# Kernel tuning notes

Hardware: AMD Instinct MI355X
Metric: run time of the kernel (lower is better)

The kernel has to match this reference:

```python
import jax, jax.numpy as jnp
import numpy as np

N = 50000          # nodes
E = 800000         # edges
F_IN, H, OUT = 512, 256, 2
BN_EPS = 1e-5


def setup_inputs() -> dict:
    key = jax.random.key(0)
    ks = jax.random.split(key, 10)
    x = jax.random.normal(ks[0], (N, F_IN), jnp.float32)
    edge_index = jax.random.randint(ks[1], (2, E), 0, N, dtype=jnp.int64)
    edge_weight = jax.random.uniform(ks[2], (E,), jnp.float32)

    def lin(k, fan_in, fan_out):
        return jax.random.normal(k, (fan_in, fan_out), jnp.float32) / np.sqrt(fan_in).astype(np.float32)

    W1, b1 = lin(ks[3], F_IN, H), jnp.zeros((H,), jnp.float32)
    W2, b2 = lin(ks[4], H, H), jnp.zeros((H,), jnp.float32)
    W3, b3 = lin(ks[5], H, OUT), jnp.zeros((OUT,), jnp.float32)
    # BatchNorm1d affine params + running stats (eval mode)
    g1, be1 = jnp.ones((H,), jnp.float32), jnp.zeros((H,), jnp.float32)
    m1 = 0.1 * jax.random.normal(ks[6], (H,), jnp.float32)
    v1 = jax.random.uniform(ks[7], (H,), jnp.float32, 0.5, 1.5)
    g2, be2 = jnp.ones((H,), jnp.float32), jnp.zeros((H,), jnp.float32)
    m2 = 0.1 * jax.random.normal(ks[8], (H,), jnp.float32)
    v2 = jax.random.uniform(ks[9], (H,), jnp.float32, 0.5, 1.5)
    return {"x": x, "edge_index": edge_index, "edge_weight": edge_weight,
            "W1": W1, "b1": b1, "g1": g1, "be1": be1, "m1": m1, "v1": v1,
            "W2": W2, "b2": b2, "g2": g2, "be2": be2, "m2": m2, "v2": v2,
            "W3": W3, "b3": b3}


def gcn_conv(x, row, col, w, W, b):
    # PyG GCNConv (eval): h = x @ W; out[col] += norm * h[row]; + b
    # row/col/w already include self-loops with weight 1.
    n = x.shape[0]
    h = x @ W                                      # [N, out]
    deg = jax.ops.segment_sum(w, col, num_segments=n)
    dinv = jnp.where(deg > 0, jax.lax.rsqrt(deg), 0.0)
    norm = dinv[row] * w * dinv[col]               # [E+N]
    out = jax.ops.segment_sum(h[row] * norm[:, None], col, num_segments=n)
    return out + b


def batchnorm_eval(x, g, be, m, v):
    return (x - m) * jax.lax.rsqrt(v + BN_EPS) * g + be


def reference(x, edge_index, edge_weight, W1, b1, g1, be1, m1, v1,
              W2, b2, g2, be2, m2, v2, W3, b3):
    n = x.shape[0]
    loops = jnp.arange(n, dtype=edge_index.dtype)
    row = jnp.concatenate([edge_index[0], loops])
    col = jnp.concatenate([edge_index[1], loops])
    w = jnp.concatenate([edge_weight, jnp.ones((n,), x.dtype)])

    h = jax.nn.relu(batchnorm_eval(gcn_conv(x, row, col, w, W1, b1), g1, be1, m1, v1))
    h = jax.nn.relu(batchnorm_eval(gcn_conv(h, row, col, w, W2, b2), g2, be2, m2, v2))
    return gcn_conv(h, row, col, w, W3, b3)
```

## Files before the change

### kernel.cpp

```cpp
#include <hip/hip_runtime.h>
#include <stdint.h>

#define F_IN 512
#define HF 256
#define OUT_F 2
#define BN_EPS 1e-5f
#define SCAN_B 256
#define LDSTR 36

typedef __attribute__((ext_vector_type(8))) short bf16x8;
typedef __attribute__((ext_vector_type(4))) float f32x4;

__device__ inline float bf2f(unsigned short u) {
    union { float f; uint32_t i; } v; v.i = ((uint32_t)u) << 16; return v.f;
}
__device__ inline unsigned short f2bf(float f) {
    union { float f; uint32_t i; } v; v.f = f;
    uint32_t r = v.i + 0x7FFFu + ((v.i >> 16) & 1u);
    return (unsigned short)(r >> 16);
}

__global__ void prep_kernel(unsigned long long* __restrict__ packed,
                            const float* __restrict__ W1, unsigned short* __restrict__ W1t,
                            const float* __restrict__ W2, unsigned short* __restrict__ W2t,
                            unsigned short* __restrict__ xbf_pad,
                            unsigned short* __restrict__ bufa_pad,
                            int n, int padx, int pada) {
    int idx = blockIdx.x * blockDim.x + threadIdx.x;
    if (idx < n) { packed[idx] = 1ULL << 20; return; }
    int j = idx - n;
    if (j < F_IN * HF) {
        int nn = j >> 9, k = j & (F_IN - 1);
        W1t[j] = f2bf(W1[(size_t)k * HF + nn]);
        return;
    }
    j -= F_IN * HF;
    if (j < HF * HF) {
        int nn = j >> 8, k = j & (HF - 1);
        W2t[j] = f2bf(W2[(size_t)k * HF + nn]);
        return;
    }
    j -= HF * HF;
    if (j < padx) { xbf_pad[j] = 0; return; }
    j -= padx;
    if (j < pada) bufa_pad[j] = 0;
}

__global__ void count_conv_kernel(const int* __restrict__ col,
                                  const float* __restrict__ w,
                                  unsigned long long* __restrict__ packed,
                                  const float* __restrict__ x,
                                  unsigned short* __restrict__ xbf,
                                  int e, int nchunk) {
    int tid = blockIdx.x * blockDim.x + threadIdx.x;
    if (tid < e) {
        unsigned long long add = (1ULL << 40)
            | (unsigned long long)__float2uint_rn(w[tid] * 1048576.0f);
        atomicAdd(&packed[col[tid]], add);
    }
    const int stride = gridDim.x * blockDim.x;
    const float4* x4 = (const float4*)x;
    for (int c = tid; c < nchunk; c += stride) {
        float4 f0 = x4[2 * c];
        float4 f1 = x4[2 * c + 1];
        bf16x8 v;
        v[0] = (short)f2bf(f0.x); v[1] = (short)f2bf(f0.y);
        v[2] = (short)f2bf(f0.z); v[3] = (short)f2bf(f0.w);
        v[4] = (short)f2bf(f1.x); v[5] = (short)f2bf(f1.y);
        v[6] = (short)f2bf(f1.z); v[7] = (short)f2bf(f1.w);
        *(bf16x8*)(xbf + (size_t)c * 8) = v;
    }
}

__global__ __launch_bounds__(256)
void gemm_kernel(const unsigned short* __restrict__ A,
                 const unsigned short* __restrict__ Bt,
                 unsigned short* __restrict__ C, int K) {
    __shared__ unsigned short As[2][128 * LDSTR];
    __shared__ unsigned short Bs[2][128 * LDSTR];
    const int tid  = threadIdx.x;
    const int lane = tid & 63;
    const int wv   = tid >> 6;
    const int wrow = wv >> 1, wcol = wv & 1;
    const int m0 = blockIdx.x * 128;
    const int n0 = blockIdx.y * 128;

    const int sr = tid >> 2;
    const int sc = (tid & 3) * 8;

    const unsigned short* pa0 = A + (size_t)(m0 + sr) * K + sc;
    const unsigned short* pa1 = A + (size_t)(m0 + sr + 64) * K + sc;
    const unsigned short* pb0 = Bt + (size_t)(n0 + sr) * K + sc;
    const unsigned short* pb1 = Bt + (size_t)(n0 + sr + 64) * K + sc;

    f32x4 zero4 = {0.0f, 0.0f, 0.0f, 0.0f};
    f32x4 acc[4][4];
    #pragma unroll
    for (int i = 0; i < 4; ++i)
        #pragma unroll
        for (int j = 0; j < 4; ++j) acc[i][j] = zero4;

    const int q8 = (lane >> 4) * 8;
    const int ml = lane & 15;

    bf16x8 va0 = *(const bf16x8*)pa0;
    bf16x8 va1 = *(const bf16x8*)pa1;
    bf16x8 vb0 = *(const bf16x8*)pb0;
    bf16x8 vb1 = *(const bf16x8*)pb1;

    const int nsteps = K >> 5;
    for (int s = 0; s < nsteps; ++s) {
        const int buf = s & 1;
        *(bf16x8*)&As[buf][sr * LDSTR + sc]        = va0;
        *(bf16x8*)&As[buf][(sr + 64) * LDSTR + sc] = va1;
        *(bf16x8*)&Bs[buf][sr * LDSTR + sc]        = vb0;
        *(bf16x8*)&Bs[buf][(sr + 64) * LDSTR + sc] = vb1;
        __syncthreads();
        if (s + 1 < nsteps) {
            int off = (s + 1) * 32;
            va0 = *(const bf16x8*)(pa0 + off);
            va1 = *(const bf16x8*)(pa1 + off);
            vb0 = *(const bf16x8*)(pb0 + off);
            vb1 = *(const bf16x8*)(pb1 + off);
        }
        bf16x8 af[4], bfr[4];
        #pragma unroll
        for (int i = 0; i < 4; ++i)
            af[i] = *(const bf16x8*)&As[buf][(wrow * 64 + i * 16 + ml) * LDSTR + q8];
        #pragma unroll
        for (int j = 0; j < 4; ++j)
            bfr[j] = *(const bf16x8*)&Bs[buf][(wcol * 64 + j * 16 + ml) * LDSTR + q8];
        #pragma unroll
        for (int i = 0; i < 4; ++i)
            #pragma unroll
            for (int j = 0; j < 4; ++j)
                acc[i][j] = __builtin_amdgcn_mfma_f32_16x16x32_bf16(af[i], bfr[j], acc[i][j], 0, 0, 0);
    }

    const int q4 = (lane >> 4) * 4;
    #pragma unroll
    for (int i = 0; i < 4; ++i) {
        #pragma unroll
        for (int j = 0; j < 4; ++j) {
            #pragma unroll
            for (int rg = 0; rg < 4; ++rg) {
                int r = m0 + wrow * 64 + i * 16 + q4 + rg;
                int c = n0 + wcol * 64 + j * 16 + ml;
                C[(size_t)r * HF + c] = f2bf(acc[i][j][rg]);
            }
        }
    }
}

__global__ void scan1_kernel(const unsigned long long* __restrict__ packed,
                             int* __restrict__ local, int* __restrict__ blocksum, int n) {
    __shared__ int tmp[SCAN_B];
    int i = blockIdx.x * SCAN_B + threadIdx.x;
    int v = (i < n) ? (int)(packed[i] >> 40) : 0;
    tmp[threadIdx.x] = v;
    __syncthreads();
    for (int off = 1; off < SCAN_B; off <<= 1) {
        int t = 0;
        if ((int)threadIdx.x >= off) t = tmp[threadIdx.x - off];
        __syncthreads();
        if ((int)threadIdx.x >= off) tmp[threadIdx.x] += t;
        __syncthreads();
    }
    if (i < n) local[i] = tmp[threadIdx.x] - v;
    if (threadIdx.x == SCAN_B - 1) blocksum[blockIdx.x] = tmp[SCAN_B - 1];
}

__global__ void scan3_dinv_kernel(int* __restrict__ csr_ptr, int* __restrict__ cursor,
                                  const int* __restrict__ blocksum,
                                  const unsigned long long* __restrict__ packed,
                                  float* __restrict__ dinv, int n, int e, int nb) {
    __shared__ int red[SCAN_B];
    int t = threadIdx.x;
    red[t] = (t < nb && t < (int)blockIdx.x) ? blocksum[t] : 0;
    __syncthreads();
    for (int off = SCAN_B / 2; off > 0; off >>= 1) {
        if (t < off) red[t] += red[t + off];
        __syncthreads();
    }
    int prefix = red[0];
    int i = blockIdx.x * SCAN_B + t;
    if (i < n) {
        int val = csr_ptr[i] + prefix;
        csr_ptr[i] = val;
        cursor[i] = val;
        float deg = (float)(packed[i] & 0xFFFFFFFFFFULL) * (1.0f / 1048576.0f);
        dinv[i] = rsqrtf(deg);
    }
    if (i == 0) csr_ptr[n] = e;
}

__global__ void fill_kernel(const int* __restrict__ row, const int* __restrict__ col,
                            const float* __restrict__ w, const float* __restrict__ dinv,
                            int* __restrict__ cursor, int2* __restrict__ csr_edge, int e) {
    int i = blockIdx.x * blockDim.x + threadIdx.x;
    if (i < e) {
        int r = row[i], c = col[i];
        int pos = atomicAdd(&cursor[c], 1);
        float nrm = dinv[r] * w[i] * dinv[c];
        csr_edge[pos] = make_int2(r, __float_as_int(nrm));
    }
}

template<int FINAL>
__global__ void agg_kernel(const unsigned short* __restrict__ h,
                           const int* __restrict__ ptr,
                           const int2* __restrict__ edge,
                           const float* __restrict__ dinv,
                           const float* __restrict__ b, const float* __restrict__ g,
                           const float* __restrict__ be, const float* __restrict__ m,
                           const float* __restrict__ v,
                           unsigned short* __restrict__ out,
                           const float* __restrict__ W3, float* __restrict__ h3, int n) {
    int wid  = (blockIdx.x * blockDim.x + threadIdx.x) >> 6;
    int lane = threadIdx.x & 63;
    if (wid >= n) return;
    int p0 = ptr[wid], p1 = ptr[wid + 1];
    const int fo = lane * 4;
    float a0 = 0.f, a1 = 0.f, a2 = 0.f, a3 = 0.f;

    const int cnt = p1 - p0;
    const int nb  = cnt >> 3;

    int2 edC[8], edN[8];
    ushort4 hvC[8];

    if (nb > 0) {
        #pragma unroll
        for (int k = 0; k < 8; ++k) edC[k] = edge[p0 + k];
        if (nb > 1) {
            #pragma unroll
            for (int k = 0; k < 8; ++k) edN[k] = edge[p0 + 8 + k];
        }
        #pragma unroll
        for (int k = 0; k < 8; ++k)
            hvC[k] = *(const ushort4*)(h + (size_t)edC[k].x * HF + fo);

        for (int bb = 0; bb < nb; ++bb) {
            ushort4 hvN[8];
            int2 edN2[8];
            if (bb + 1 < nb) {
                if (bb + 2 < nb) {
                    int pp = p0 + (bb + 2) * 8;
                    #pragma unroll
                    for (int k = 0; k < 8; ++k) edN2[k] = edge[pp + k];
                }
                #pragma unroll
                for (int k = 0; k < 8; ++k)
                    hvN[k] = *(const ushort4*)(h + (size_t)edN[k].x * HF + fo);
            }
            #pragma unroll
            for (int k = 0; k < 8; ++k) {
                float nw = __int_as_float(edC[k].y);
                a0 += nw * bf2f(hvC[k].x);
                a1 += nw * bf2f(hvC[k].y);
                a2 += nw * bf2f(hvC[k].z);
                a3 += nw * bf2f(hvC[k].w);
            }
            #pragma unroll
            for (int k = 0; k < 8; ++k) { edC[k] = edN[k]; edN[k] = edN2[k]; hvC[k] = hvN[k]; }
        }
    }
    const int pend = p0 + nb * 8;
    if (pend < p1) {
        int2 ed[8];
        float wv[8];
        #pragma unroll
        for (int k = 0; k < 8; ++k) {
            int idx = pend + k < p1 ? pend + k : p1 - 1;
            ed[k] = edge[idx];
            wv[k] = (pend + k < p1) ? __int_as_float(ed[k].y) : 0.0f;
        }
        ushort4 hv[8];
        #pragma unroll
        for (int k = 0; k < 8; ++k)
            hv[k] = *(const ushort4*)(h + (size_t)ed[k].x * HF + fo);
        #pragma unroll
        for (int k = 0; k < 8; ++k) {
            a0 += wv[k] * bf2f(hv[k].x);
            a1 += wv[k] * bf2f(hv[k].y);
            a2 += wv[k] * bf2f(hv[k].z);
            a3 += wv[k] * bf2f(hv[k].w);
        }
    }
    float s = dinv[wid];
    float sl = s * s;
    ushort4 hv = *(const ushort4*)(h + (size_t)wid * HF + fo);
    a0 += sl * bf2f(hv.x);
    a1 += sl * bf2f(hv.y);
    a2 += sl * bf2f(hv.z);
    a3 += sl * bf2f(hv.w);

    float4 bb  = *(const float4*)(b + fo);
    float4 gg  = *(const float4*)(g + fo);
    float4 bee = *(const float4*)(be + fo);
    float4 mm  = *(const float4*)(m + fo);
    float4 vv  = *(const float4*)(v + fo);
    float f0 = fmaxf((a0 + bb.x - mm.x) * rsqrtf(vv.x + BN_EPS) * gg.x + bee.x, 0.f);
    float f1 = fmaxf((a1 + bb.y - mm.y) * rsqrtf(vv.y + BN_EPS) * gg.y + bee.y, 0.f);
    float f2 = fmaxf((a2 + bb.z - mm.z) * rsqrtf(vv.z + BN_EPS) * gg.z + bee.z, 0.f);
    float f3 = fmaxf((a3 + bb.w - mm.w) * rsqrtf(vv.w + BN_EPS) * gg.w + bee.w, 0.f);

    if (!FINAL) {
        ushort4 o;
        o.x = f2bf(f0); o.y = f2bf(f1); o.z = f2bf(f2); o.w = f2bf(f3);
        *(ushort4*)(out + (size_t)wid * HF + fo) = o;
    } else {
        float4 w0 = *(const float4*)(W3 + fo * 2);
        float4 w1 = *(const float4*)(W3 + fo * 2 + 4);
        float s0 = f0 * w0.x + f1 * w0.z + f2 * w1.x + f3 * w1.z;
        float s1 = f0 * w0.y + f1 * w0.w + f2 * w1.y + f3 * w1.w;
        #pragma unroll
        for (int o = 32; o > 0; o >>= 1) {
            s0 += __shfl_down(s0, o, 64);
            s1 += __shfl_down(s1, o, 64);
        }
        if (lane == 0) {
            h3[wid * 2 + 0] = s0;
            h3[wid * 2 + 1] = s1;
        }
    }
}

__global__ void out_kernel(const float* __restrict__ h3,
                           const int* __restrict__ ptr, const int2* __restrict__ edge,
                           const float* __restrict__ dinv,
                           const float* __restrict__ b3, float* __restrict__ out, int n) {
    int i = blockIdx.x * blockDim.x + threadIdx.x;
    if (i >= n) return;
    int p0 = ptr[i], p1 = ptr[i + 1];
    float a0 = 0.f, a1 = 0.f;
    for (int p = p0; p < p1; p += 4) {
        #pragma unroll
        for (int k = 0; k < 4; ++k) {
            int idx = p + k < p1 ? p + k : p1 - 1;
            int2 e = edge[idx];
            float nw = (p + k < p1) ? __int_as_float(e.y) : 0.0f;
            float2 u = *(const float2*)(h3 + 2 * e.x);
            a0 += nw * u.x;
            a1 += nw * u.y;
        }
    }
    float s = dinv[i];
    float sl = s * s;
    out[2 * i + 0] = a0 + sl * h3[2 * i + 0] + b3[0];
    out[2 * i + 1] = a1 + sl * h3[2 * i + 1] + b3[1];
}

static inline char* align16(char* p) {
    return (char*)(((uintptr_t)p + 15) & ~(uintptr_t)15);
}

extern "C" void kernel_launch(void* const* d_in, const int* in_sizes, int n_in,
                              void* d_out, int out_size, void* d_ws, size_t ws_size,
                              hipStream_t stream) {
    const float* x   = (const float*)d_in[0];
    const int*   ei  = (const int*)d_in[1];
    const float* ew  = (const float*)d_in[2];
    const float* W1  = (const float*)d_in[3];
    const float* b1  = (const float*)d_in[4];
    const float* g1  = (const float*)d_in[5];
    const float* be1 = (const float*)d_in[6];
    const float* m1  = (const float*)d_in[7];
    const float* v1  = (const float*)d_in[8];
    const float* W2  = (const float*)d_in[9];
    const float* b2  = (const float*)d_in[10];
    const float* g2  = (const float*)d_in[11];
    const float* be2 = (const float*)d_in[12];
    const float* m2  = (const float*)d_in[13];
    const float* v2  = (const float*)d_in[14];
    const float* W3  = (const float*)d_in[15];
    const float* b3  = (const float*)d_in[16];

    const int N  = in_sizes[0] / F_IN;
    const int E  = in_sizes[2];
    const int MP = (N + 127) & ~127;
    const int* row = ei;
    const int* col = ei + E;

    char* wsb = (char*)d_ws;
    unsigned long long* packed = (unsigned long long*)wsb; wsb = align16(wsb + (size_t)N * 8);
    float* dinv     = (float*)wsb;          wsb = align16(wsb + (size_t)N * 4);
    int*   csr_ptr  = (int*)wsb;            wsb = align16(wsb + (size_t)(N + 1) * 4);
    int*   cursor   = (int*)wsb;            wsb = align16(wsb + (size_t)N * 4);
    int*   blocksum = (int*)wsb;            wsb = align16(wsb + (size_t)SCAN_B * 4);
    int2*  csr_edge = (int2*)wsb;           wsb = align16(wsb + (size_t)E * 8);
    unsigned short* W1t = (unsigned short*)wsb;  wsb = align16(wsb + (size_t)F_IN * HF * 2);
    unsigned short* W2t = (unsigned short*)wsb;  wsb = align16(wsb + (size_t)HF * HF * 2);
    unsigned short* xbf  = (unsigned short*)wsb; wsb = align16(wsb + (size_t)MP * F_IN * 2);
    unsigned short* bufh = (unsigned short*)wsb; wsb = align16(wsb + (size_t)MP * HF * 2);
    unsigned short* bufa = (unsigned short*)wsb; wsb = align16(wsb + (size_t)MP * HF * 2);
    float* h3 = (float*)wsb;                wsb = align16(wsb + (size_t)N * OUT_F * 4);
    float* outf = (float*)d_out;

    const int TB = 256;
    const int nscan = (N + SCAN_B - 1) / SCAN_B;
    const int padx = (MP - N) * F_IN;
    const int pada = (MP - N) * HF;
    const int preptot = N + F_IN * HF + HF * HF + padx + pada;
    const int ncc = (E + TB - 1) / TB;
    const int nchunk = (N * F_IN) / 8;

    prep_kernel<<<(preptot + TB - 1) / TB, TB, 0, stream>>>(
        packed, W1, W1t, W2, W2t, xbf + (size_t)N * F_IN, bufa + (size_t)N * HF, N, padx, pada);

    count_conv_kernel<<<ncc, TB, 0, stream>>>(col, ew, packed, x, xbf, E, nchunk);

    scan1_kernel<<<nscan, SCAN_B, 0, stream>>>(packed, csr_ptr, blocksum, N);
    scan3_dinv_kernel<<<nscan, SCAN_B, 0, stream>>>(csr_ptr, cursor, blocksum, packed, dinv, N, E, nscan);
    fill_kernel<<<(E + TB - 1) / TB, TB, 0, stream>>>(row, col, ew, dinv, cursor, csr_edge, E);

    dim3 ggrid(MP / 128, HF / 128);

    gemm_kernel<<<ggrid, TB, 0, stream>>>(xbf, W1t, bufh, F_IN);
    agg_kernel<0><<<((size_t)N * 64 + TB - 1) / TB, TB, 0, stream>>>(
        bufh, csr_ptr, csr_edge, dinv, b1, g1, be1, m1, v1, bufa, nullptr, nullptr, N);

    gemm_kernel<<<ggrid, TB, 0, stream>>>(bufa, W2t, bufh, HF);
    agg_kernel<1><<<((size_t)N * 64 + TB - 1) / TB, TB, 0, stream>>>(
        bufh, csr_ptr, csr_edge, dinv, b2, g2, be2, m2, v2, nullptr, W3, h3, N);

    out_kernel<<<(N + TB - 1) / TB, TB, 0, stream>>>(h3, csr_ptr, csr_edge, dinv, b3, outf, N);
}
```

Before: 471.1 us.

## Fuse CSR fill with first GEMM and fold prep into count kernel

Removes the separate prep kernel. Weight transposes and pad zeroing move into grid-stride loops inside the count/convert kernel, and the packed-degree init becomes a memset, with the self-loop degree of 1 added back in the dinv computation. The CSR fill and the first GEMM now run in one launch with a block-index split, so the independent fill blocks and GEMM tiles can overlap. This saves two launches and fills idle CUs, at the cost of shared-memory allocation for the fill blocks and a possible imbalance in block scheduling.

```diff
diff --git a/kernel.cpp b/kernel.cpp
--- a/kernel.cpp
+++ b/kernel.cpp
@@ -20,45 +20,23 @@
     return (unsigned short)(r >> 16);
 }
 
-__global__ void prep_kernel(unsigned long long* __restrict__ packed,
-                            const float* __restrict__ W1, unsigned short* __restrict__ W1t,
-                            const float* __restrict__ W2, unsigned short* __restrict__ W2t,
-                            unsigned short* __restrict__ xbf_pad,
-                            unsigned short* __restrict__ bufa_pad,
-                            int n, int padx, int pada) {
-    int idx = blockIdx.x * blockDim.x + threadIdx.x;
-    if (idx < n) { packed[idx] = 1ULL << 20; return; }
-    int j = idx - n;
-    if (j < F_IN * HF) {
-        int nn = j >> 9, k = j & (F_IN - 1);
-        W1t[j] = f2bf(W1[(size_t)k * HF + nn]);
-        return;
-    }
-    j -= F_IN * HF;
-    if (j < HF * HF) {
-        int nn = j >> 8, k = j & (HF - 1);
-        W2t[j] = f2bf(W2[(size_t)k * HF + nn]);
-        return;
-    }
-    j -= HF * HF;
-    if (j < padx) { xbf_pad[j] = 0; return; }
-    j -= padx;
-    if (j < pada) bufa_pad[j] = 0;
-}
-
 __global__ void count_conv_kernel(const int* __restrict__ col,
                                   const float* __restrict__ w,
                                   unsigned long long* __restrict__ packed,
                                   const float* __restrict__ x,
                                   unsigned short* __restrict__ xbf,
-                                  int e, int nchunk) {
+                                  const float* __restrict__ W1, unsigned short* __restrict__ W1t,
+                                  const float* __restrict__ W2, unsigned short* __restrict__ W2t,
+                                  unsigned short* __restrict__ xbf_pad,
+                                  unsigned short* __restrict__ bufa_pad,
+                                  int e, int nchunk, int padx, int pada) {
     int tid = blockIdx.x * blockDim.x + threadIdx.x;
+    const int stride = gridDim.x * blockDim.x;
     if (tid < e) {
         unsigned long long add = (1ULL << 40)
             | (unsigned long long)__float2uint_rn(w[tid] * 1048576.0f);
         atomicAdd(&packed[col[tid]], add);
     }
-    const int stride = gridDim.x * blockDim.x;
     const float4* x4 = (const float4*)x;
     for (int c = tid; c < nchunk; c += stride) {
         float4 f0 = x4[2 * c];
@@ -70,20 +48,71 @@
         v[6] = (short)f2bf(f1.z); v[7] = (short)f2bf(f1.w);
         *(bf16x8*)(xbf + (size_t)c * 8) = v;
     }
-}
-
-__global__ __launch_bounds__(256)
-void gemm_kernel(const unsigned short* __restrict__ A,
-                 const unsigned short* __restrict__ Bt,
-                 unsigned short* __restrict__ C, int K) {
-    __shared__ unsigned short As[2][128 * LDSTR];
-    __shared__ unsigned short Bs[2][128 * LDSTR];
+    for (int j = tid; j < F_IN * HF; j += stride) {
+        int nn = j >> 9, k = j & (F_IN - 1);
+        W1t[j] = f2bf(W1[(size_t)k * HF + nn]);
+    }
+    for (int j = tid; j < HF * HF; j += stride) {
+        int nn = j >> 8, k = j & (HF - 1);
+        W2t[j] = f2bf(W2[(size_t)k * HF + nn]);
+    }
+    for (int j = tid; j < padx; j += stride) xbf_pad[j] = 0;
+    for (int j = tid; j < pada; j += stride) bufa_pad[j] = 0;
+}
+
+__global__ void scan1_kernel(const unsigned long long* __restrict__ packed,
+                             int* __restrict__ local, int* __restrict__ blocksum, int n) {
+    __shared__ int tmp[SCAN_B];
+    int i = blockIdx.x * SCAN_B + threadIdx.x;
+    int v = (i < n) ? (int)(packed[i] >> 40) : 0;
+    tmp[threadIdx.x] = v;
+    __syncthreads();
+    for (int off = 1; off < SCAN_B; off <<= 1) {
+        int t = 0;
+        if ((int)threadIdx.x >= off) t = tmp[threadIdx.x - off];
+        __syncthreads();
+        if ((int)threadIdx.x >= off) tmp[threadIdx.x] += t;
+        __syncthreads();
+    }
+    if (i < n) local[i] = tmp[threadIdx.x] - v;
+    if (threadIdx.x == SCAN_B - 1) blocksum[blockIdx.x] = tmp[SCAN_B - 1];
+}
+
+__global__ void scan3_dinv_kernel(int* __restrict__ csr_ptr, int* __restrict__ cursor,
+                                  const int* __restrict__ blocksum,
+                                  const unsigned long long* __restrict__ packed,
+                                  float* __restrict__ dinv, int n, int e, int nb) {
+    __shared__ int red[SCAN_B];
+    int t = threadIdx.x;
+    red[t] = (t < nb && t < (int)blockIdx.x) ? blocksum[t] : 0;
+    __syncthreads();
+    for (int off = SCAN_B / 2; off > 0; off >>= 1) {
+        if (t < off) red[t] += red[t + off];
+        __syncthreads();
+    }
+    int prefix = red[0];
+    int i = blockIdx.x * SCAN_B + t;
+    if (i < n) {
+        int val = csr_ptr[i] + prefix;
+        csr_ptr[i] = val;
+        cursor[i] = val;
+        float deg = 1.0f + (float)(packed[i] & 0xFFFFFFFFFFULL) * (1.0f / 1048576.0f);
+        dinv[i] = rsqrtf(deg);
+    }
+    if (i == 0) csr_ptr[n] = e;
+}
+
+__device__ __forceinline__
+void gemm_body(const unsigned short* __restrict__ A,
+               const unsigned short* __restrict__ Bt,
+               unsigned short* __restrict__ C, int K, int mblk, int nblk,
+               unsigned short (*As)[128 * LDSTR], unsigned short (*Bs)[128 * LDSTR]) {
     const int tid  = threadIdx.x;
     const int lane = tid & 63;
     const int wv   = tid >> 6;
     const int wrow = wv >> 1, wcol = wv & 1;
-    const int m0 = blockIdx.x * 128;
-    const int n0 = blockIdx.y * 128;
+    const int m0 = mblk * 128;
+    const int n0 = nblk * 128;
 
     const int sr = tid >> 2;
     const int sc = (tid & 3) * 8;
@@ -152,58 +181,37 @@
     }
 }
 
-__global__ void scan1_kernel(const unsigned long long* __restrict__ packed,
-                             int* __restrict__ local, int* __restrict__ blocksum, int n) {
-    __shared__ int tmp[SCAN_B];
-    int i = blockIdx.x * SCAN_B + threadIdx.x;
-    int v = (i < n) ? (int)(packed[i] >> 40) : 0;
-    tmp[threadIdx.x] = v;
-    __syncthreads();
-    for (int off = 1; off < SCAN_B; off <<= 1) {
-        int t = 0;
-        if ((int)threadIdx.x >= off) t = tmp[threadIdx.x - off];
-        __syncthreads();
-        if ((int)threadIdx.x >= off) tmp[threadIdx.x] += t;
-        __syncthreads();
-    }
-    if (i < n) local[i] = tmp[threadIdx.x] - v;
-    if (threadIdx.x == SCAN_B - 1) blocksum[blockIdx.x] = tmp[SCAN_B - 1];
-}
-
-__global__ void scan3_dinv_kernel(int* __restrict__ csr_ptr, int* __restrict__ cursor,
-                                  const int* __restrict__ blocksum,
-                                  const unsigned long long* __restrict__ packed,
-                                  float* __restrict__ dinv, int n, int e, int nb) {
-    __shared__ int red[SCAN_B];
-    int t = threadIdx.x;
-    red[t] = (t < nb && t < (int)blockIdx.x) ? blocksum[t] : 0;
-    __syncthreads();
-    for (int off = SCAN_B / 2; off > 0; off >>= 1) {
-        if (t < off) red[t] += red[t + off];
-        __syncthreads();
-    }
-    int prefix = red[0];
-    int i = blockIdx.x * SCAN_B + t;
-    if (i < n) {
-        int val = csr_ptr[i] + prefix;
-        csr_ptr[i] = val;
-        cursor[i] = val;
-        float deg = (float)(packed[i] & 0xFFFFFFFFFFULL) * (1.0f / 1048576.0f);
-        dinv[i] = rsqrtf(deg);
-    }
-    if (i == 0) csr_ptr[n] = e;
-}
-
-__global__ void fill_kernel(const int* __restrict__ row, const int* __restrict__ col,
-                            const float* __restrict__ w, const float* __restrict__ dinv,
-                            int* __restrict__ cursor, int2* __restrict__ csr_edge, int e) {
-    int i = blockIdx.x * blockDim.x + threadIdx.x;
-    if (i < e) {
-        int r = row[i], c = col[i];
-        int pos = atomicAdd(&cursor[c], 1);
-        float nrm = dinv[r] * w[i] * dinv[c];
-        csr_edge[pos] = make_int2(r, __float_as_int(nrm));
-    }
+__global__ __launch_bounds__(256)
+void fill_gemm1_kernel(const int* __restrict__ row, const int* __restrict__ col,
+                       const float* __restrict__ w, const float* __restrict__ dinv,
+                       int* __restrict__ cursor, int2* __restrict__ csr_edge, int e,
+                       const unsigned short* __restrict__ A,
+                       const unsigned short* __restrict__ Bt,
+                       unsigned short* __restrict__ C, int nfill) {
+    __shared__ unsigned short As[2][128 * LDSTR];
+    __shared__ unsigned short Bs[2][128 * LDSTR];
+    int bid = blockIdx.x;
+    if (bid < nfill) {
+        int i = bid * 256 + (int)threadIdx.x;
+        if (i < e) {
+            int r = row[i], c = col[i];
+            int pos = atomicAdd(&cursor[c], 1);
+            float nrm = dinv[r] * w[i] * dinv[c];
+            csr_edge[pos] = make_int2(r, __float_as_int(nrm));
+        }
+    } else {
+        int gb = bid - nfill;
+        gemm_body(A, Bt, C, F_IN, gb >> 1, gb & 1, As, Bs);
+    }
+}
+
+__global__ __launch_bounds__(256)
+void gemm_kernel(const unsigned short* __restrict__ A,
+                 const unsigned short* __restrict__ Bt,
+                 unsigned short* __restrict__ C, int K) {
+    __shared__ unsigned short As[2][128 * LDSTR];
+    __shared__ unsigned short Bs[2][128 * LDSTR];
+    gemm_body(A, Bt, C, K, blockIdx.x, blockIdx.y, As, Bs);
 }
 
 template<int FINAL>
@@ -401,26 +409,29 @@
     const int nscan = (N + SCAN_B - 1) / SCAN_B;
     const int padx = (MP - N) * F_IN;
     const int pada = (MP - N) * HF;
-    const int preptot = N + F_IN * HF + HF * HF + padx + pada;
     const int ncc = (E + TB - 1) / TB;
     const int nchunk = (N * F_IN) / 8;
-
-    prep_kernel<<<(preptot + TB - 1) / TB, TB, 0, stream>>>(
-        packed, W1, W1t, W2, W2t, xbf + (size_t)N * F_IN, bufa + (size_t)N * HF, N, padx, pada);
-
-    count_conv_kernel<<<ncc, TB, 0, stream>>>(col, ew, packed, x, xbf, E, nchunk);
+    const int nfill = (E + TB - 1) / TB;
+    const int ngemm = (MP / 128) * 2;
+
+    hipMemsetAsync(packed, 0, (size_t)N * 8, stream);
+
+    count_conv_kernel<<<ncc, TB, 0, stream>>>(
+        col, ew, packed, x, xbf, W1, W1t, W2, W2t,
+        xbf + (size_t)N * F_IN, bufa + (size_t)N * HF, E, nchunk, padx, pada);
 
     scan1_kernel<<<nscan, SCAN_B, 0, stream>>>(packed, csr_ptr, blocksum, N);
     scan3_dinv_kernel<<<nscan, SCAN_B, 0, stream>>>(csr_ptr, cursor, blocksum, packed, dinv, N, E, nscan);
-    fill_kernel<<<(E + TB - 1) / TB, TB, 0, stream>>>(row, col, ew, dinv, cursor, csr_edge, E);
-
-    dim3 ggrid(MP / 128, HF / 128);
-
-    gemm_kernel<<<ggrid, TB, 0, stream>>>(xbf, W1t, bufh, F_IN);
+
+    fill_gemm1_kernel<<<nfill + ngemm, TB, 0, stream>>>(
+        row, col, ew, dinv, cursor, csr_edge, E, xbf, W1t, bufh, nfill);
+
     agg_kernel<0><<<((size_t)N * 64 + TB - 1) / TB, TB, 0, stream>>>(
         bufh, csr_ptr, csr_edge, dinv, b1, g1, be1, m1, v1, bufa, nullptr, nullptr, N);
 
+    dim3 ggrid(MP / 128, HF / 128);
     gemm_kernel<<<ggrid, TB, 0, stream>>>(bufa, W2t, bufh, HF);
+
     agg_kernel<1><<<((size_t)N * 64 + TB - 1) / TB, TB, 0, stream>>>(
         bufh, csr_ptr, csr_edge, dinv, b2, g2, be2, m2, v2, nullptr, W3, h3, N);
 
```

Measured after the change: 533.3 us. 1.13x slower.
